# Performance work log

Hardware: AMD Instinct MI355X
Metric: run time of the kernel (lower is better)

## Reference

```python
import jax, jax.numpy as jnp
import numpy as np

MAP_X = 72; MAP_Y = 72      # global map grid
R = 300                      # number of rooms
MAXS = 8                     # rooms padded to 8x8 (zero-padded occupancy)
E = 32                       # room_embedding_width
N = 128                      # batch
CONV_CH = [64, 128, 256]; KS = [5, 3, 3]
FC = [512, 256]; OUT_W = 512


def setup_inputs() -> dict:
    key = jax.random.key(0)
    ks = jax.random.split(key, 20)
    rng = np.random.default_rng(0)
    widths = rng.integers(1, MAXS + 1, R)
    heights = rng.integers(1, MAXS + 1, R)
    # room_maps[i] is room.map transposed -> [width, height], zero-padded to [MAXS, MAXS]
    rm = np.zeros((R, MAXS, MAXS), np.int32)
    for i in range(R):
        rm[i, :widths[i], :heights[i]] = rng.integers(0, 2, (int(widths[i]), int(heights[i])))
    inp = {}
    # room top-left positions; rooms fit since max size is MAXS
    inp["X"] = jax.random.randint(ks[0], (N, R, 2), 0, MAP_X - MAXS + 1, dtype=jnp.int32)
    inp["room_maps"] = jnp.asarray(rm)
    inp["room_emb"] = jax.random.normal(ks[1], (R, E), jnp.float32)
    cin = [1 + E] + CONV_CH
    for i in range(3):
        k = KS[i]; fan = cin[i] * k * k
        inp[f"conv_w{i}"] = jax.random.normal(ks[2 + 2 * i], (cin[i + 1], cin[i], k, k), jnp.float32) / np.sqrt(fan).astype(np.float32)
        inp[f"conv_b{i}"] = jnp.zeros((cin[i + 1],), jnp.float32)
    fcd = [CONV_CH[-1]] + FC + [OUT_W]
    for i in range(3):
        inp[f"fc_w{i}"] = jax.random.normal(ks[10 + 2 * i], (fcd[i + 1], fcd[i]), jnp.float32) / np.sqrt(fcd[i]).astype(np.float32)
        inp[f"fc_b{i}"] = jnp.zeros((fcd[i + 1],), jnp.float32)
    return inp


def _encode_map(X, room_maps, room_emb):
    # Fused scatter: occupancy channel + embedding channels scattered in one pass.
    rm = room_maps.astype(room_emb.dtype)                    # [R, W, H]
    vals = jnp.concatenate(
        [rm[..., None], rm[..., None] * room_emb[:, None, None, :]], axis=-1
    )                                                        # [R, W, H, 1+E]
    ax = jnp.arange(MAXS)

    def one(pos):  # pos: [R, 2] positions for one batch element
        ix = jnp.broadcast_to(pos[:, 0, None, None] + ax[None, :, None], (R, MAXS, MAXS))
        iy = jnp.broadcast_to(pos[:, 1, None, None] + ax[None, None, :], (R, MAXS, MAXS))
        grid = jnp.zeros((MAP_X, MAP_Y, 1 + E), vals.dtype)
        # padded cells are zero so dropped/duplicate adds are exact
        return grid.at[ix, iy].add(vals, mode="drop")

    out = jax.vmap(one)(X)                                   # [N, MAP_X, MAP_Y, 1+E]
    # torch: transpose(1,3) -> [N, 1+E, MAP_Y, MAP_X]
    return jnp.transpose(out, (0, 3, 2, 1))


def _conv_relu(x, w, b, k):
    p = k // 2
    y = jax.lax.conv_general_dilated(
        x, w, (1, 1), [(p, p), (p, p)], dimension_numbers=("NCHW", "OIHW", "NCHW"))
    return jax.nn.relu(y + b[None, :, None, None])


def _maxpool3s2(x):
    return jax.lax.reduce_window(x, -jnp.inf, jax.lax.max, (1, 1, 3, 3), (1, 1, 2, 2), "VALID")


def reference(X, room_maps, room_emb, conv_w0, conv_b0, conv_w1, conv_b1, conv_w2, conv_b2, fc_w0, fc_b0, fc_w1, fc_b1, fc_w2, fc_b2):
    x = _encode_map(X, room_maps, room_emb)
    for w, b, k in ((conv_w0, conv_b0, KS[0]), (conv_w1, conv_b1, KS[1]), (conv_w2, conv_b2, KS[2])):
        x = _maxpool3s2(_conv_relu(x, w, b, k))
    x = jnp.mean(x, axis=(2, 3))                             # GlobalAvgPool2d
    x = jax.nn.relu(x @ fc_w0.T + fc_b0)
    x = jax.nn.relu(x @ fc_w1.T + fc_b1)
    return x @ fc_w2.T + fc_b2
```

## Files before the change

kernel.cpp:

```cpp
#include <hip/hip_runtime.h>
#include <hip/hip_bf16.h>
#include <cstdint>
#include <cstddef>

#define NB      128
#define RR      300
#define EMB     32

typedef __bf16 bf16x8 __attribute__((ext_vector_type(8)));
typedef float  f32x4  __attribute__((ext_vector_type(4)));
typedef unsigned short ushort8 __attribute__((ext_vector_type(8)));

__device__ __forceinline__ unsigned short f2bf(float f) {
    union { __hip_bfloat16 h; unsigned short u; } c;
    c.h = __float2bfloat16(f);
    return c.u;
}
__device__ __forceinline__ float bf2f(unsigned short u) {
    union { __hip_bfloat16 h; unsigned short u; } c;
    c.u = u;
    return __bfloat162float(c.h);
}

__device__ __forceinline__ void wpack_body(
    const float* __restrict__ w, unsigned short* __restrict__ wPT,
    int COUT, int CIN, int KK, int gpc, int idx, int total)
{
    if (idx >= total) return;
    int kk = idx & 31;
    int t  = idx >> 5;
    int oc = t % COUT;
    int kb = t / COUT;
    int g  = kb * 4 + (kk >> 3);
    int j  = kk & 7;
    int shift = g / gpc;
    int ci    = (g % gpc) * 8 + j;
    float v = (shift < KK && ci < CIN)
        ? w[(size_t)oc * CIN * KK + (size_t)ci * KK + shift] : 0.0f;
    wPT[idx] = f2bf(v);
}

__device__ __forceinline__ void fcT_body(
    const float* __restrict__ w, float* __restrict__ wT, int O, int I, int idx)
{
    if (idx >= O * I) return;
    int i = idx % I, o = idx / I;
    wT[(size_t)i * O + o] = w[idx];
}

__global__ __launch_bounds__(256) void prep_k(
    const int* __restrict__ rm, unsigned long long* __restrict__ masks,
    const float* __restrict__ cw0, unsigned short* __restrict__ WP0,
    const float* __restrict__ cw1, unsigned short* __restrict__ WP1,
    const float* __restrict__ cw2, unsigned short* __restrict__ WP2,
    int* __restrict__ kt0, int* __restrict__ kt1, int* __restrict__ kt2,
    const float* __restrict__ fw0, float* __restrict__ W0T,
    const float* __restrict__ fw1, float* __restrict__ W1T,
    const float* __restrict__ fw2, float* __restrict__ W2T)
{
    const int b = blockIdx.x;
    const int t = threadIdx.x;
    if (b < 2) {
        int r = b * 256 + t;
        if (r < RR) {
            unsigned long long m = 0ull;
            #pragma unroll
            for (int k = 0; k < 64; ++k)
                if (rm[r * 64 + k]) m |= (1ull << k);
            masks[r] = m;
        }
    } else if (b < 258) {
        wpack_body(cw0, WP0, 64, 33, 25, 5, (b - 2) * 256 + t, 32 * 64 * 32);
    } else if (b < 546) {
        wpack_body(cw1, WP1, 128, 64, 9, 8, (b - 258) * 256 + t, 18 * 128 * 32);
    } else if (b < 1698) {
        wpack_body(cw2, WP2, 256, 128, 9, 16, (b - 546) * 256 + t, 36 * 256 * 32);
    } else if (b < 1699) {
        #pragma unroll
        for (int which = 0; which < 3; ++which) {
            int ngr, gpc, K, Wp, CL;
            int* dst;
            if (which == 0)      { ngr = 128; gpc = 5;  K = 5; Wp = 20; CL = 40;  dst = kt0; }
            else if (which == 1) { ngr = 72;  gpc = 8;  K = 3; Wp = 37; CL = 72;  dst = kt1; }
            else                 { ngr = 144; gpc = 16; K = 3; Wp = 19; CL = 136; dst = kt2; }
            if (t < ngr) {
                int shift = t / gpc;
                int off = 0;
                if (shift < K * K) {
                    int ky = shift / K, kx = shift % K;
                    off = (ky * Wp + kx) * CL + (t % gpc) * 8;
                }
                dst[t] = off;
            }
        }
    } else if (b < 2211) {
        fcT_body(fw0, W0T, 512, 256, (b - 1699) * 256 + t);
    } else if (b < 2723) {
        fcT_body(fw1, W1T, 256, 512, (b - 2211) * 256 + t);
    } else {
        fcT_body(fw2, W2T, 512, 256, (b - 2723) * 256 + t);
    }
}

__device__ __forceinline__ void border_body(
    unsigned short* __restrict__ base, int Hp, int Wp, int CPG, int pad,
    int sampleStride, int nborder, int idx, int total)
{
    if (idx >= total) return;
    int c8 = idx % CPG;
    int t  = idx / CPG;
    int bi = t % nborder;
    int nl = t / nborder;

    int topN = pad * Wp;
    int y, x;
    if (bi < topN) {
        y = bi / Wp; x = bi - y * Wp;
    } else if (bi < 2 * topN) {
        int b2 = bi - topN;
        y = Hp - pad + b2 / Wp; x = b2 % Wp;
    } else {
        int mid = bi - 2 * topN;
        int rowlen = 2 * pad;
        y = pad + mid / rowlen;
        int r = mid % rowlen;
        x = r < pad ? r : Wp - pad + (r - pad);
    }
    uint4 z = make_uint4(0, 0, 0, 0);
    *reinterpret_cast<uint4*>(
        &base[((size_t)nl * sampleStride) +
              ((size_t)y * Wp + x) * (CPG * 8) + c8 * 8]) = z;
}

__global__ __launch_bounds__(512) void encode_k(
    const int* __restrict__ X, const unsigned long long* __restrict__ masks,
    const float* __restrict__ emb, unsigned short* __restrict__ G,
    int n0, int sampleStride)
{
    __shared__ float tile[4][72][33];
    __shared__ unsigned s_pos[RR];
    __shared__ unsigned long long s_mask[RR];
    __shared__ unsigned short s_list[320];
    __shared__ float s_emb[64 * 33];
    __shared__ int s_woff[8];
    __shared__ int s_cnt;

    const int nl = blockIdx.x, band = blockIdx.y;
    const int by = band * 4;
    const int n  = n0 + nl;
    const int tid = threadIdx.x;

    float* tf = &tile[0][0][0];
    for (int i = tid; i < 4 * 72 * 33; i += 512) tf[i] = 0.0f;

    const int2* Xp = reinterpret_cast<const int2*>(X);
    bool hot = false;
    if (tid < RR) {
        int2 pos = Xp[n * RR + tid];
        s_pos[tid]  = (unsigned)pos.x | ((unsigned)pos.y << 16);
        s_mask[tid] = masks[tid];
        hot = (pos.y <= by + 3) && (pos.y + 7 >= by);
    }
    unsigned long long bal = __ballot(hot);
    if ((tid & 63) == 0) s_woff[tid >> 6] = (int)__popcll(bal);
    __syncthreads();
    if (tid == 0) {
        int acc = 0;
        #pragma unroll
        for (int w = 0; w < 8; ++w) { int c = s_woff[w]; s_woff[w] = acc; acc += c; }
        s_cnt = acc;
    }
    __syncthreads();
    if (hot) {
        int w = tid >> 6, b = tid & 63;
        unsigned long long before = (b == 0) ? 0ull : (bal & ((1ull << b) - 1ull));
        s_list[s_woff[w] + (int)__popcll(before)] = (unsigned short)tid;
    }
    __syncthreads();

    const int lane = tid & 63;
    const int wvi  = tid >> 6;
    const int dx   = lane >> 3;
    const int c0   = (lane & 7) * 5;
    const int cnt  = s_cnt;

    for (int base = 0; base < cnt; base += 64) {
        int cn = cnt - base; if (cn > 64) cn = 64;
        for (int i = tid; i < cn * 33; i += 512) {
            int hi = i / 33, cc = i - hi * 33;
            int r = s_list[base + hi];
            s_emb[i] = (cc == 0) ? 1.0f : emb[r * EMB + cc - 1];
        }
        __syncthreads();

        int j = wvi;
        for (; j + 8 < cn; j += 16) {
            int rA = s_list[base + j];
            int rB = s_list[base + j + 8];
            unsigned pA = s_pos[rA], pB = s_pos[rB];
            unsigned long long mA = s_mask[rA] >> (dx * 8);
            unsigned long long mB = s_mask[rB] >> (dx * 8);
            int xA = (pA & 0xffff) + dx, yA = pA >> 16;
            int xB = (pB & 0xffff) + dx, yB = pB >> 16;
            float eA[5], eB[5];
            #pragma unroll
            for (int q = 0; q < 5; ++q) {
                eA[q] = (c0 + q < 33) ? s_emb[j * 33 + c0 + q] : 0.0f;
                eB[q] = (c0 + q < 33) ? s_emb[(j + 8) * 33 + c0 + q] : 0.0f;
            }
            #pragma unroll
            for (int dyb = 0; dyb < 4; ++dyb) {
                int dA = by + dyb - yA;
                if ((unsigned)dA < 8u && ((mA >> dA) & 1ull)) {
                    #pragma unroll
                    for (int q = 0; q < 5; ++q)
                        if (c0 + q < 33)
                            atomicAdd(&tile[dyb][xA][c0 + q], eA[q]);
                }
                int dB = by + dyb - yB;
                if ((unsigned)dB < 8u && ((mB >> dB) & 1ull)) {
                    #pragma unroll
                    for (int q = 0; q < 5; ++q)
                        if (c0 + q < 33)
                            atomicAdd(&tile[dyb][xB][c0 + q], eB[q]);
                }
            }
        }
        for (; j < cn; j += 8) {
            int r = s_list[base + j];
            unsigned pxy = s_pos[r];
            int px = pxy & 0xffff, py = pxy >> 16;
            unsigned long long mm = s_mask[r] >> (dx * 8);
            int x = px + dx;
            float ev[5];
            #pragma unroll
            for (int q = 0; q < 5; ++q)
                ev[q] = (c0 + q < 33) ? s_emb[j * 33 + c0 + q] : 0.0f;
            #pragma unroll
            for (int dyb = 0; dyb < 4; ++dyb) {
                int dyr = by + dyb - py;
                if ((unsigned)dyr < 8u && ((mm >> dyr) & 1ull)) {
                    #pragma unroll
                    for (int q = 0; q < 5; ++q)
                        if (c0 + q < 33)
                            atomicAdd(&tile[dyb][x][c0 + q], ev[q]);
                }
            }
        }
        __syncthreads();
    }
    __syncthreads();

    unsigned short* Gn = G + (size_t)nl * sampleStride;
    for (int i = tid; i < 4 * 72 * 10; i += 512) {
        int cc = i % 10;
        int t  = i / 10;
        int x  = t % 72;
        int dyb = t / 72;
        int c0w = cc * 4;
        unsigned short r[4];
        #pragma unroll
        for (int j = 0; j < 4; ++j)
            r[j] = (c0w + j < 33) ? f2bf(tile[dyb][x][c0w + j]) : 0;
        uint2 pk;
        pk.x = (unsigned)r[0] | ((unsigned)r[1] << 16);
        pk.y = (unsigned)r[2] | ((unsigned)r[3] << 16);
        *reinterpret_cast<uint2*>(
            &Gn[((size_t)(by + dyb + 2) * 76 + (x + 2)) * 40 + c0w]) = pk;
    }

    uint2 zz; zz.x = 0; zz.y = 0;
    for (int i = tid; i < 160; i += 512) {
        int cc = i % 10;
        int t  = i / 10;
        int ci = t & 3;
        int dyb = t >> 2;
        int x = ci < 2 ? ci : 72 + ci;
        *reinterpret_cast<uint2*>(
            &Gn[((size_t)(by + dyb + 2) * 76 + x) * 40 + cc * 4]) = zz;
    }
    if (band == 0 || band == 17) {
        int rbase = band == 0 ? 0 : 74;
        for (int i = tid; i < 2 * 76 * 10; i += 512) {
            int cc = i % 10;
            int t  = i / 10;
            int x  = t % 76;
            int r  = t / 76;
            *reinterpret_cast<uint2*>(
                &Gn[((size_t)(rbase + r) * 76 + x) * 40 + cc * 4]) = zz;
        }
    }
}

template<int KSTEPS>
__global__ __launch_bounds__(256, 3) void conv0_tile_k(
    const unsigned short* __restrict__ inP,
    const unsigned short* __restrict__ wPT,
    const int* __restrict__ ktab,
    const float* __restrict__ bias,
    unsigned short* __restrict__ out,
    int inSS, int outSS)
{
    constexpr int CL = 40;
    constexpr int LP = 72;
    __shared__ __align__(16) unsigned short slab[28 * 20 * CL];
    __shared__ int s_kt[KSTEPS * 4];
    unsigned short* s_c = slab;

    const int tid = threadIdx.x;
    const int tl  = blockIdx.x;
    const int nl  = blockIdx.y;
    const int tyi = tl / 5, txi = tl % 5;
    const int y0 = tyi * 24;
    const int x0 = txi < 4 ? txi * 16 : 56;

    const int lane = tid & 63, wv = tid >> 6, frow = lane & 15, fq = lane >> 4;

    if (tid < KSTEPS * 4) s_kt[tid] = ktab[tid];

    const unsigned short* in_n = inP + (size_t)nl * inSS;
    {
        const uint4* src = reinterpret_cast<const uint4*>(in_n);
        uint4* dst = reinterpret_cast<uint4*>(slab);
        #pragma unroll
        for (int it = 0; it < 11; ++it) {
            int q = tid + it * 256;
            if (q < 2800) {
                int r = q / 100, c = q - r * 100;
                dst[q] = src[((y0 + r) * 76 + x0) * 5 + c];
            }
        }
    }

    int ldsb[6];
    #pragma unroll
    for (int mf = 0; mf < 6; ++mf)
        ldsb[mf] = ((mf * 4 + wv) * 20 + frow) * CL;

    const unsigned short* wbase = wPT + (size_t)frow * 32 + fq * 8;

    f32x4 acc[6][4];
    #pragma unroll
    for (int a = 0; a < 6; ++a)
        #pragma unroll
        for (int b = 0; b < 4; ++b) acc[a][b] = (f32x4){0.f, 0.f, 0.f, 0.f};

    __syncthreads();

    #pragma unroll 2
    for (int kb = 0; kb < KSTEPS; ++kb) {
        int go = s_kt[kb * 4 + fq];
        bf16x8 af[6];
        #pragma unroll
        for (int mf = 0; mf < 6; ++mf)
            af[mf] = *reinterpret_cast<const bf16x8*>(&slab[ldsb[mf] + go]);
        const unsigned short* wk = wbase + (size_t)kb * 64 * 32;
        #pragma unroll
        for (int ng = 0; ng < 4; ++ng) {
            bf16x8 bf = *reinterpret_cast<const bf16x8*>(wk + ng * 16 * 32);
            #pragma unroll
            for (int mf = 0; mf < 6; ++mf)
                acc[mf][ng] = __builtin_amdgcn_mfma_f32_16x16x32_bf16(
                    af[mf], bf, acc[mf][ng], 0, 0, 0);
        }
    }

    unsigned short* out_n = out + (size_t)nl * outSS;
    const int erow = tid >> 2, eseg = tid & 3;
    #pragma unroll
    for (int mf = 0; mf < 6; ++mf) {
        __syncthreads();
        #pragma unroll
        for (int ng = 0; ng < 4; ++ng) {
            float bv = bias[ng * 16 + frow];
            #pragma unroll
            for (int j = 0; j < 4; ++j)
                s_c[(wv * 16 + fq * 4 + j) * LP + ng * 16 + frow] =
                    f2bf(fmaxf(acc[mf][ng][j] + bv, 0.0f));
        }
        __syncthreads();
        {
            int ty = mf * 4 + (erow >> 4);
            int tx = erow & 15;
            int pos = (y0 + ty) * 72 + (x0 + tx);
            ushort8 v0 = *reinterpret_cast<const ushort8*>(
                &s_c[erow * LP + eseg * 16]);
            ushort8 v1 = *reinterpret_cast<const ushort8*>(
                &s_c[erow * LP + eseg * 16 + 8]);
            unsigned short* op = out_n + (size_t)pos * 64 + eseg * 16;
            *reinterpret_cast<ushort8*>(op) = v0;
            *reinterpret_cast<ushort8*>(op + 8) = v1;
        }
    }
}

template<int MFRAG, int NG, int KH, int CPG, int CL, int SLAB, int KSTEPS>
__global__ __launch_bounds__(256, 2) void conv_mfma_k(
    const unsigned short* __restrict__ inP,
    const unsigned short* __restrict__ wPT,
    const int* __restrict__ ktab,
    const float* __restrict__ bias,
    unsigned short* __restrict__ out,
    int W, int Wp, int Mtot, int inSS, int outSS, int COUT)
{
    constexpr int Mblk = MFRAG * 64;
    constexpr int NOC  = NG * 16;
    constexpr int SEGS = NOC / 16;
    constexpr int LP   = NOC + 8;
    constexpr int CP   = CPG * 8;
    constexpr int SMEM = (SLAB * 2 > 64 * LP * 2) ? SLAB * 2 : 64 * LP * 2;
    __shared__ __align__(16) char smem[SMEM];
    __shared__ int s_kt[KSTEPS * 4];
    unsigned short* slab = reinterpret_cast<unsigned short*>(smem);
    unsigned short* s_c  = reinterpret_cast<unsigned short*>(smem);

    const int tid  = threadIdx.x;
    const int mb   = blockIdx.x;
    const int ocb  = blockIdx.y;
    const int nl   = blockIdx.z;
    const int lane = tid & 63;
    const int wv   = tid >> 6;
    const int frow = lane & 15;
    const int fq   = lane >> 4;

    if (tid < KSTEPS * 4) s_kt[tid] = ktab[tid];

    const int p0    = mb * Mblk;
    const int y0    = p0 / W;
    const int plast = (p0 + Mblk < Mtot ? p0 + Mblk : Mtot) - 1;
    const int rows  = plast / W - y0 + KH;

    const unsigned short* in_n =
        inP + (size_t)nl * inSS + (size_t)y0 * Wp * CP;
    const int nchunks = rows * Wp * CPG;
    for (int q = tid; q < nchunks; q += 256) {
        int pix = q / CPG, c8 = q - pix * CPG;
        uint4 v = reinterpret_cast<const uint4*>(in_n)[q];
        *reinterpret_cast<uint4*>(&slab[pix * CL + c8 * 8]) = v;
    }

    int ldsb[MFRAG];
    #pragma unroll
    for (int mf = 0; mf < MFRAG; ++mf) {
        int p  = p0 + mf * 64 + wv * 16 + frow;
        int pc = p < Mtot ? p : (Mtot - 1);
        int y  = pc / W;
        int x  = pc - y * W;
        ldsb[mf] = ((y - y0) * Wp + x) * CL;
    }
    const unsigned short* wbase =
        wPT + ((size_t)(ocb * NOC + frow)) * 32 + fq * 8;

    f32x4 acc[MFRAG][NG];
    #pragma unroll
    for (int mf = 0; mf < MFRAG; ++mf)
        #pragma unroll
        for (int ng = 0; ng < NG; ++ng)
            acc[mf][ng] = (f32x4){0.f, 0.f, 0.f, 0.f};

    __syncthreads();

    for (int kb = 0; kb < KSTEPS; ++kb) {
        int go = s_kt[kb * 4 + fq];
        bf16x8 af[MFRAG];
        #pragma unroll
        for (int mf = 0; mf < MFRAG; ++mf)
            af[mf] = *reinterpret_cast<const bf16x8*>(&slab[ldsb[mf] + go]);
        const unsigned short* wk = wbase + (size_t)kb * COUT * 32;
        #pragma unroll
        for (int ng = 0; ng < NG; ++ng) {
            bf16x8 bf = *reinterpret_cast<const bf16x8*>(wk + ng * 16 * 32);
            #pragma unroll
            for (int mf = 0; mf < MFRAG; ++mf)
                acc[mf][ng] = __builtin_amdgcn_mfma_f32_16x16x32_bf16(
                    af[mf], bf, acc[mf][ng], 0, 0, 0);
        }
    }

    unsigned short* out_n = out + (size_t)nl * outSS;
    #pragma unroll
    for (int mf = 0; mf < MFRAG; ++mf) {
        __syncthreads();
        #pragma unroll
        for (int ng = 0; ng < NG; ++ng) {
            float bv = bias[ocb * NOC + ng * 16 + frow];
            #pragma unroll
            for (int j = 0; j < 4; ++j)
                s_c[(wv * 16 + fq * 4 + j) * LP + ng * 16 + frow] =
                    f2bf(fmaxf(acc[mf][ng][j] + bv, 0.0f));
        }
        __syncthreads();
        for (int t = tid; t < 64 * SEGS; t += 256) {
            int row = t / SEGS, seg = t % SEGS;
            int p = p0 + mf * 64 + row;
            if (p < Mtot) {
                ushort8 v0 = *reinterpret_cast<const ushort8*>(
                    &s_c[row * LP + seg * 16]);
                ushort8 v1 = *reinterpret_cast<const ushort8*>(
                    &s_c[row * LP + seg * 16 + 8]);
                unsigned short* op =
                    out_n + (size_t)p * COUT + ocb * NOC + seg * 16;
                *reinterpret_cast<ushort8*>(op) = v0;
                *reinterpret_cast<ushort8*>(op + 8) = v1;
            }
        }
    }
}

__global__ __launch_bounds__(256) void pool_border_k(
    const unsigned short* __restrict__ in, unsigned short* __restrict__ out,
    int CG, int C, int W, int inSS,
    int HO, int WO, int Wpo, int outSS, int total,
    int npool, int bHp, int bWp, int bCPG, int bpad, int bnborder, int btotal)
{
    const int b = blockIdx.x;
    const int tidx = threadIdx.x;
    if (b >= npool) {
        border_body(out, bHp, bWp, bCPG, bpad, outSS, bnborder,
                    (b - npool) * 256 + tidx, btotal);
        return;
    }
    int idx = b * 256 + tidx;
    if (idx >= total) return;
    int cg = idx % CG;
    int t  = idx / CG;
    int x  = t % WO;
    t /= WO;
    int y  = t % HO;
    int nl = t / HO;

    const unsigned short* pin = in + (size_t)nl * inSS + cg * 8;
    ushort8 mx = {0,0,0,0,0,0,0,0};
    #pragma unroll
    for (int dy = 0; dy < 3; ++dy)
        #pragma unroll
        for (int dx = 0; dx < 3; ++dx) {
            ushort8 v = *reinterpret_cast<const ushort8*>(
                pin + ((size_t)(2 * y + dy) * W + (2 * x + dx)) * C);
            #pragma unroll
            for (int j = 0; j < 8; ++j) mx[j] = v[j] > mx[j] ? v[j] : mx[j];
        }
    *reinterpret_cast<ushort8*>(
        out + (size_t)nl * outSS +
        ((size_t)(y + 1) * Wpo + (x + 1)) * C + cg * 8) = mx;
}

__global__ __launch_bounds__(256) void pool2gap_k(
    const unsigned short* __restrict__ in, float* __restrict__ out,
    int inSS, int n0)
{
    __shared__ float red[4][4][8];
    const int nl = blockIdx.x;
    const int cg = blockIdx.y;
    const int tid = threadIdx.x;
    const int w  = tid >> 2;
    const int cq = tid & 3;
    const int y = w >> 3, x = w & 7;

    const unsigned short* p = in + (size_t)nl * inSS + cg * 32 + cq * 8;
    ushort8 mx = {0,0,0,0,0,0,0,0};
    #pragma unroll
    for (int dy = 0; dy < 3; ++dy)
        #pragma unroll
        for (int dx = 0; dx < 3; ++dx) {
            ushort8 v = *reinterpret_cast<const ushort8*>(
                p + ((size_t)(2 * y + dy) * 17 + (2 * x + dx)) * 256);
            #pragma unroll
            for (int j = 0; j < 8; ++j) mx[j] = v[j] > mx[j] ? v[j] : mx[j];
        }
    float s[8];
    #pragma unroll
    for (int j = 0; j < 8; ++j) s[j] = bf2f(mx[j]);
    #pragma unroll
    for (int m = 4; m < 64; m <<= 1)
        #pragma unroll
        for (int j = 0; j < 8; ++j)
            s[j] += __shfl_xor(s[j], m);
    if ((tid & 63) < 4) {
        #pragma unroll
        for (int j = 0; j < 8; ++j) red[tid >> 6][tid & 3][j] = s[j];
    }
    __syncthreads();
    if (tid < 32) {
        int cq2 = tid >> 3, j = tid & 7;
        float t = red[0][cq2][j] + red[1][cq2][j] + red[2][cq2][j] + red[3][cq2][j];
        out[(size_t)(n0 + nl) * 256 + cg * 32 + cq2 * 8 + j] = t * (1.0f / 64.0f);
    }
}

__global__ __launch_bounds__(256) void fc_fused_k(
    const float* __restrict__ in,
    const float* __restrict__ w0T, const float* __restrict__ b0,
    const float* __restrict__ w1T, const float* __restrict__ b1,
    const float* __restrict__ w2T, const float* __restrict__ b2,
    float* __restrict__ out)
{
    __shared__ float s_in[256], s_h0[512], s_h1[256];
    const int n = blockIdx.x, t = threadIdx.x;
    s_in[t] = in[(size_t)n * 256 + t];
    __syncthreads();
    float a0 = 0.f, a1 = 0.f;
    for (int i = 0; i < 256; ++i) {
        float v = s_in[i];
        a0 += v * w0T[i * 512 + t];
        a1 += v * w0T[i * 512 + t + 256];
    }
    s_h0[t]       = fmaxf(a0 + b0[t], 0.0f);
    s_h0[t + 256] = fmaxf(a1 + b0[t + 256], 0.0f);
    __syncthreads();
    float h = 0.f;
    for (int i = 0; i < 512; ++i) h += s_h0[i] * w1T[i * 256 + t];
    s_h1[t] = fmaxf(h + b1[t], 0.0f);
    __syncthreads();
    a0 = 0.f; a1 = 0.f;
    for (int i = 0; i < 256; ++i) {
        float v = s_h1[i];
        a0 += v * w2T[i * 512 + t];
        a1 += v * w2T[i * 512 + t + 256];
    }
    out[(size_t)n * 512 + t]       = a0 + b2[t];
    out[(size_t)n * 512 + t + 256] = a1 + b2[t + 256];
}

extern "C" void kernel_launch(void* const* d_in, const int* in_sizes, int n_in,
                              void* d_out, int out_size, void* d_ws, size_t ws_size,
                              hipStream_t stream)
{
    const int*   X   = (const int*)d_in[0];
    const int*   rm  = (const int*)d_in[1];
    const float* emb = (const float*)d_in[2];
    const float* cw0 = (const float*)d_in[3];
    const float* cb0 = (const float*)d_in[4];
    const float* cw1 = (const float*)d_in[5];
    const float* cb1 = (const float*)d_in[6];
    const float* cw2 = (const float*)d_in[7];
    const float* cb2 = (const float*)d_in[8];
    const float* fw0 = (const float*)d_in[9];
    const float* fb0 = (const float*)d_in[10];
    const float* fw1 = (const float*)d_in[11];
    const float* fb1 = (const float*)d_in[12];
    const float* fw2 = (const float*)d_in[13];
    const float* fb2 = (const float*)d_in[14];
    float* out = (float*)d_out;

    char* p = (char*)d_ws;
    auto alloc = [&](size_t bytes) -> char* {
        char* r = p; p += (bytes + 255) & ~(size_t)255; return r;
    };
    unsigned short* WP0 = (unsigned short*)alloc((size_t)32 * 64 * 32 * 2);
    unsigned short* WP1 = (unsigned short*)alloc((size_t)18 * 128 * 32 * 2);
    unsigned short* WP2 = (unsigned short*)alloc((size_t)36 * 256 * 32 * 2);
    int* KT0 = (int*)alloc(128 * 4);
    int* KT1 = (int*)alloc(72 * 4);
    int* KT2 = (int*)alloc(144 * 4);
    unsigned long long* MASKS = (unsigned long long*)alloc(RR * 8);
    float* W0T  = (float*)alloc((size_t)256 * 512 * 4);
    float* W1T  = (float*)alloc((size_t)512 * 256 * 4);
    float* W2T  = (float*)alloc((size_t)256 * 512 * 4);
    float* GAPB = (float*)alloc((size_t)NB * 256 * 4);
    size_t fixed_bytes = (size_t)(p - (char*)d_ws);

    const size_t A_FL = 231040, B_FL = 331776, C_FL = 133824;
    const size_t per_sample = (A_FL + B_FL + C_FL) * 2 + 768;
    int Bc = 128;
    while (Bc > 1 && fixed_bytes + (size_t)Bc * per_sample > ws_size) Bc >>= 1;

    unsigned short* bufA = (unsigned short*)alloc((size_t)Bc * A_FL * 2);
    unsigned short* bufC = (unsigned short*)alloc((size_t)Bc * C_FL * 2);
    unsigned short* bufB = (unsigned short*)alloc((size_t)Bc * B_FL * 2);

    prep_k<<<3235, 256, 0, stream>>>(
        rm, MASKS, cw0, WP0, cw1, WP1, cw2, WP2,
        KT0, KT1, KT2, fw0, W0T, fw1, W1T, fw2, W2T);

    for (int n0 = 0; n0 < NB; n0 += Bc) {
        encode_k<<<dim3(Bc, 18), 512, 0, stream>>>(X, MASKS, emb, bufA, n0, (int)A_FL);

        conv0_tile_k<32><<<dim3(15, Bc), 256, 0, stream>>>(
            bufA, WP0, KT0, cb0, bufB, (int)A_FL, (int)B_FL);

        {
            int total = Bc * 35 * 35 * 8;
            int npool = (total + 255) / 256;
            int btotal = Bc * 144 * 8;
            int nbord = (btotal + 255) / 256;
            pool_border_k<<<npool + nbord, 256, 0, stream>>>(
                bufB, bufC, 8, 64, 72, (int)B_FL,
                35, 35, 37, (int)C_FL, total,
                npool, 37, 37, 8, 1, 144, btotal);
        }

        conv_mfma_k<4, 8, 3, 8, 72, 29304, 18><<<dim3(5, 1, Bc), 256, 0, stream>>>(
            bufC, WP1, KT1, cb1, bufA, 35, 37,
            1225, (int)C_FL, (int)A_FL, 128);

        {
            int total = Bc * 17 * 17 * 16;
            int npool = (total + 255) / 256;
            int btotal = Bc * 72 * 16;
            int nbord = (btotal + 255) / 256;
            pool_border_k<<<npool + nbord, 256, 0, stream>>>(
                bufA, bufC + 87616, 16, 128, 35, (int)A_FL,
                17, 17, 19, (int)C_FL, total,
                npool, 19, 19, 16, 1, 72, btotal);
        }

        conv_mfma_k<5, 8, 3, 16, 136, 49096, 36><<<dim3(1, 2, Bc), 256, 0, stream>>>(
            bufC + 87616, WP2, KT2, cb2, bufB, 17, 19,
            289, (int)C_FL, (int)B_FL, 256);

        pool2gap_k<<<dim3(Bc, 8), 256, 0, stream>>>(bufB, GAPB, (int)B_FL, n0);
    }

    fc_fused_k<<<NB, 256, 0, stream>>>(GAPB, W0T, fb0, W1T, fb1, W2T, fb2, out);
}
```

Baseline: 466.7 us.

## Double-buffer conv0 weights in LDS via async loads; batch conv epilogue stores

In conv0, each K-step's weight tile is now prefetched into a double-buffered LDS region with global_load_lds while the current step's MFMAs run. The B fragments are read from LDS instead of directly from global memory. In the generic conv kernel, the epilogue stages all M fragments into a larger shared buffer before one store pass, which removes the per-fragment sync pairs. The costs are a __syncthreads per K-step in conv0, extra LDS that may lower occupancy, and a larger epilogue buffer in the generic conv kernel.

After: 458.0 us. Within noise of the previous version (-1.9%).

```diff
diff --git a/kernel.cpp b/kernel.cpp
--- a/kernel.cpp
+++ b/kernel.cpp
@@ -304,6 +304,7 @@
     constexpr int CL = 40;
     constexpr int LP = 72;
     __shared__ __align__(16) unsigned short slab[28 * 20 * CL];
+    __shared__ __align__(16) unsigned short wbuf[2][2048];
     __shared__ int s_kt[KSTEPS * 4];
     unsigned short* s_c = slab;
 
@@ -318,6 +319,14 @@
 
     if (tid < KSTEPS * 4) s_kt[tid] = ktab[tid];
 
+    {
+        const unsigned short* src = wPT + wv * 512 + lane * 8;
+        __builtin_amdgcn_global_load_lds(
+            (const __attribute__((address_space(1))) void*)src,
+            (__attribute__((address_space(3))) void*)&wbuf[0][wv * 512],
+            16, 0, 0);
+    }
+
     const unsigned short* in_n = inP + (size_t)nl * inSS;
     {
         const uint4* src = reinterpret_cast<const uint4*>(in_n);
@@ -337,8 +346,6 @@
     for (int mf = 0; mf < 6; ++mf)
         ldsb[mf] = ((mf * 4 + wv) * 20 + frow) * CL;
 
-    const unsigned short* wbase = wPT + (size_t)frow * 32 + fq * 8;
-
     f32x4 acc[6][4];
     #pragma unroll
     for (int a = 0; a < 6; ++a)
@@ -349,20 +356,30 @@
 
     #pragma unroll 2
     for (int kb = 0; kb < KSTEPS; ++kb) {
+        const int cur = kb & 1;
+        if (kb + 1 < KSTEPS) {
+            const unsigned short* src =
+                wPT + (size_t)(kb + 1) * 2048 + wv * 512 + lane * 8;
+            __builtin_amdgcn_global_load_lds(
+                (const __attribute__((address_space(1))) void*)src,
+                (__attribute__((address_space(3))) void*)&wbuf[cur ^ 1][wv * 512],
+                16, 0, 0);
+        }
         int go = s_kt[kb * 4 + fq];
         bf16x8 af[6];
         #pragma unroll
         for (int mf = 0; mf < 6; ++mf)
             af[mf] = *reinterpret_cast<const bf16x8*>(&slab[ldsb[mf] + go]);
-        const unsigned short* wk = wbase + (size_t)kb * 64 * 32;
+        const unsigned short* wl = &wbuf[cur][frow * 32 + fq * 8];
         #pragma unroll
         for (int ng = 0; ng < 4; ++ng) {
-            bf16x8 bf = *reinterpret_cast<const bf16x8*>(wk + ng * 16 * 32);
+            bf16x8 bf = *reinterpret_cast<const bf16x8*>(&wl[ng * 512]);
             #pragma unroll
             for (int mf = 0; mf < 6; ++mf)
                 acc[mf][ng] = __builtin_amdgcn_mfma_f32_16x16x32_bf16(
                     af[mf], bf, acc[mf][ng], 0, 0, 0);
         }
+        __syncthreads();
     }
 
     unsigned short* out_n = out + (size_t)nl * outSS;
@@ -408,7 +425,8 @@
     constexpr int SEGS = NOC / 16;
     constexpr int LP   = NOC + 8;
     constexpr int CP   = CPG * 8;
-    constexpr int SMEM = (SLAB * 2 > 64 * LP * 2) ? SLAB * 2 : 64 * LP * 2;
+    constexpr int CSZ  = Mblk * LP * 2;
+    constexpr int SMEM = (SLAB * 2 > CSZ) ? SLAB * 2 : CSZ;
     __shared__ __align__(16) char smem[SMEM];
     __shared__ int s_kt[KSTEPS * 4];
     unsigned short* slab = reinterpret_cast<unsigned short*>(smem);
@@ -477,32 +495,32 @@
         }
     }
 
-    unsigned short* out_n = out + (size_t)nl * outSS;
+    __syncthreads();
     #pragma unroll
     for (int mf = 0; mf < MFRAG; ++mf) {
-        __syncthreads();
         #pragma unroll
         for (int ng = 0; ng < NG; ++ng) {
             float bv = bias[ocb * NOC + ng * 16 + frow];
             #pragma unroll
             for (int j = 0; j < 4; ++j)
-                s_c[(wv * 16 + fq * 4 + j) * LP + ng * 16 + frow] =
+                s_c[(mf * 64 + wv * 16 + fq * 4 + j) * LP + ng * 16 + frow] =
                     f2bf(fmaxf(acc[mf][ng][j] + bv, 0.0f));
         }
-        __syncthreads();
-        for (int t = tid; t < 64 * SEGS; t += 256) {
-            int row = t / SEGS, seg = t % SEGS;
-            int p = p0 + mf * 64 + row;
-            if (p < Mtot) {
-                ushort8 v0 = *reinterpret_cast<const ushort8*>(
-                    &s_c[row * LP + seg * 16]);
-                ushort8 v1 = *reinterpret_cast<const ushort8*>(
-                    &s_c[row * LP + seg * 16 + 8]);
-                unsigned short* op =
-                    out_n + (size_t)p * COUT + ocb * NOC + seg * 16;
-                *reinterpret_cast<ushort8*>(op) = v0;
-                *reinterpret_cast<ushort8*>(op + 8) = v1;
-            }
+    }
+    __syncthreads();
+    unsigned short* out_n = out + (size_t)nl * outSS;
+    for (int t = tid; t < Mblk * SEGS; t += 256) {
+        int row = t / SEGS, seg = t - row * SEGS;
+        int p = p0 + row;
+        if (p < Mtot) {
+            ushort8 v0 = *reinterpret_cast<const ushort8*>(
+                &s_c[row * LP + seg * 16]);
+            ushort8 v1 = *reinterpret_cast<const ushort8*>(
+                &s_c[row * LP + seg * 16 + 8]);
+            unsigned short* op =
+                out_n + (size_t)p * COUT + ocb * NOC + seg * 16;
+            *reinterpret_cast<ushort8*>(op) = v0;
+            *reinterpret_cast<ushort8*>(op + 8) = v1;
         }
     }
 }
```
